# Performance work log

Hardware: AMD Instinct MI355X
Metric: run time of the kernel (lower is better)

The kernel has to match this reference:

```python
import jax, jax.numpy as jnp
import numpy as np

B, T, D, H, K = 2, 1024, 1024, 4096, 8


def setup_inputs() -> dict:
    key = jax.random.key(0)
    ks = jax.random.split(key, 5)
    x = jax.random.normal(ks[0], (B, T, D), dtype=jnp.float32)
    # hard one-hot routing weights per token (no learned router)
    expert_ids = jax.random.randint(ks[1], (B, T), 0, K)
    combine_weights = jax.nn.one_hot(expert_ids, K, dtype=jnp.float32)
    scale_in = 1.0 / np.sqrt(D)
    scale_h = 1.0 / np.sqrt(H)
    wg = jax.random.normal(ks[2], (K, D, H), dtype=jnp.float32) * scale_in
    wu = jax.random.normal(ks[3], (K, D, H), dtype=jnp.float32) * scale_in
    wd = jax.random.normal(ks[4], (K, H, D), dtype=jnp.float32) * scale_h
    return {"x": x, "combine_weights": combine_weights, "wg": wg, "wu": wu, "wd": wd}


def reference(x, combine_weights, wg, wu, wd):
    # Each expert is a SwiGLU FFN: down( silu(gate(x)) * up(x) ).
    # Dense baseline: every token runs through all K experts (as in source).
    g = jnp.einsum('btd,kdh->btkh', x, wg)          # [B,T,K,H]
    u = jnp.einsum('btd,kdh->btkh', x, wu)          # [B,T,K,H]
    h = jax.nn.silu(g) * u                          # [B,T,K,H]
    expert_outs = jnp.einsum('btkh,khd->btkd', h, wd)  # [B,T,K,D]
    y = jnp.einsum('btk,btkd->btd', combine_weights, expert_outs)
    return y.astype(x.dtype)
```

## Files before the change

### kernel.cpp

```cpp
#include <hip/hip_runtime.h>

typedef __attribute__((ext_vector_type(8))) short bf16x8;
typedef __attribute__((ext_vector_type(4))) float f32x4;
typedef unsigned short u16;

#define NTOK 2048
#define DDIM 1024
#define HDIM 4096
#define KEXP 8

#define BM 320
#define BK 64
#define NDESC 16

__device__ __forceinline__ u16 f2bf(float f) {
  union { float f; unsigned int u; } c; c.f = f;
  unsigned int u = c.u;
  return (u16)((u + 0x7FFFu + ((u >> 16) & 1u)) >> 16);
}
__device__ __forceinline__ unsigned pk2(float a, float b) {
  return (unsigned)f2bf(a) | ((unsigned)f2bf(b) << 16);
}

#define BAR() do { \
  asm volatile("s_waitcnt lgkmcnt(0)" ::: "memory"); \
  __builtin_amdgcn_sched_barrier(0); \
  __builtin_amdgcn_s_barrier(); \
  __builtin_amdgcn_sched_barrier(0); \
} while (0)

__global__ void route_kernel(const float* __restrict__ cw, int* __restrict__ offs,
                             int* __restrict__ perm, float* __restrict__ wsel,
                             int* __restrict__ desc) {
  __shared__ int cnt[KEXP];
  __shared__ int base[KEXP];
  const int t = threadIdx.x;
  if (t < KEXP) cnt[t] = 0;
  __syncthreads();
  int eid[8]; float wv[8];
  #pragma unroll
  for (int i = 0; i < 8; i++) {
    const int tok = t * 8 + i;
    const float* p = cw + tok * KEXP;
    int best = 0; float bw = p[0];
    #pragma unroll
    for (int k = 1; k < KEXP; k++) { float v = p[k]; if (v > bw) { bw = v; best = k; } }
    eid[i] = best; wv[i] = bw;
    atomicAdd(&cnt[best], 1);
  }
  __syncthreads();
  if (t == 0) {
    int s = 0, nd = 0;
    for (int k = 0; k < KEXP; k++) {
      const int ck = cnt[k];
      base[k] = s; offs[k] = s;
      for (int m0 = 0; m0 < ck && nd < NDESC; m0 += BM)
        desc[nd++] = (k << 12) | (s + m0);
      s += ck;
    }
    offs[KEXP] = s;
    for (; nd < NDESC; nd++) desc[nd] = -1;
  }
  __syncthreads();
  #pragma unroll
  for (int i = 0; i < 8; i++) {
    const int tok = t * 8 + i;
    const int pos = atomicAdd(&base[eid[i]], 1);
    perm[pos] = tok;
    wsel[pos] = wv[i];
  }
}

__global__ void gather_x(const float* __restrict__ x, const int* __restrict__ perm,
                         u16* __restrict__ Xb) {
  const int slot = blockIdx.x;
  const int tok = perm[slot];
  const int t = threadIdx.x;
  float4 v = ((const float4*)(x + (size_t)tok * DDIM))[t];
  ushort4 o; o.x = f2bf(v.x); o.y = f2bf(v.y); o.z = f2bf(v.z); o.w = f2bf(v.w);
  ((ushort4*)(Xb + (size_t)slot * DDIM))[t] = o;
}

__global__ __launch_bounds__(1024, 4) void gemm_swiglu(
    const u16* __restrict__ Xb,
    const float* __restrict__ wg, const float* __restrict__ wu,
    const int* __restrict__ offs, const int* __restrict__ desc,
    u16* __restrict__ Hb) {
  __shared__ u16 As[2][BM * 64];
  __shared__ u16 Bs[2][2][64 * 64];

  const int d = desc[blockIdx.y];
  if (d < 0) return;
  const int e = d >> 12;
  const int slot0 = d & 0xFFF;
  const int Msub = offs[e + 1] - slot0;
  const int n0 = blockIdx.x * 64;

  const int t = threadIdx.x;
  const int lane = t & 63;
  const int W = t >> 6;
  const int wm = W >> 2;
  const int wn = W & 3;
  const int l15 = lane & 15;
  const int lhi = lane >> 4;

  const bool do_a = t < 640;
  const int a_row = t >> 1;
  const int a_c0 = (t & 1) * 4;
  const u16* a_src = Xb + (size_t)min(slot0 + a_row, NTOK - 1) * DDIM + a_c0 * 8;
  const int a_swz = a_row & 7;

  const int tb = t & 511;
  const int matsel = t >> 9;
  const float* b_base = (matsel ? wu : wg) + (size_t)e * DDIM * HDIM;
  const int b_n = tb & 63;
  const int b_c = tb >> 6;
  const float* b_src = b_base + (size_t)(b_c * 8) * HDIM + n0 + b_n;
  const int b_off = b_n * 64 + ((b_c ^ (b_n & 7)) << 3);

  float bR[8];
  f32x4 accg[5] = {};
  f32x4 accu[5] = {};

  #define LOADB(tile) { const float* p_ = b_src + (size_t)(tile) * BK * HDIM; \
    _Pragma("unroll") for (int j = 0; j < 8; j++) bR[j] = p_[(size_t)j * HDIM]; }
  #define WRITEB(buf) { uint4 w_; \
    w_.x = pk2(bR[0], bR[1]); w_.y = pk2(bR[2], bR[3]); \
    w_.z = pk2(bR[4], bR[5]); w_.w = pk2(bR[6], bR[7]); \
    *(uint4*)(&Bs[buf][matsel][b_off]) = w_; }
  #define STAGE(buf, tA, tBnext, doB) { \
    uint4 a0_ = {}, a1_ = {}, a2_ = {}, a3_ = {}; \
    if (do_a) { const uint4* p_ = (const uint4*)(a_src + (tA) * BK); \
      a0_ = p_[0]; a1_ = p_[1]; a2_ = p_[2]; a3_ = p_[3]; } \
    WRITEB(buf); \
    if (doB) LOADB(tBnext); \
    if (do_a) { u16* base_ = &As[buf][a_row * 64]; \
      *(uint4*)(base_ + (((a_c0 + 0) ^ a_swz) << 3)) = a0_; \
      *(uint4*)(base_ + (((a_c0 + 1) ^ a_swz) << 3)) = a1_; \
      *(uint4*)(base_ + (((a_c0 + 2) ^ a_swz) << 3)) = a2_; \
      *(uint4*)(base_ + (((a_c0 + 3) ^ a_swz) << 3)) = a3_; } \
  }
  #define COMPUTE(buf) { _Pragma("unroll") for (int ks = 0; ks < 2; ks++) { \
      const int cx_ = (((ks << 2) + lhi) ^ (l15 & 7)) << 3; \
      bf16x8 bg_ = *(const bf16x8*)(&Bs[buf][0][(wn * 16 + l15) * 64] + cx_); \
      bf16x8 bu_ = *(const bf16x8*)(&Bs[buf][1][(wn * 16 + l15) * 64] + cx_); \
      _Pragma("unroll") for (int fm = 0; fm < 5; fm++) { \
        bf16x8 af_ = *(const bf16x8*)(&As[buf][(wm * 80 + fm * 16 + l15) * 64] + cx_); \
        accg[fm] = __builtin_amdgcn_mfma_f32_16x16x32_bf16(af_, bg_, accg[fm], 0, 0, 0); \
        accu[fm] = __builtin_amdgcn_mfma_f32_16x16x32_bf16(af_, bu_, accu[fm], 0, 0, 0); } } }

  LOADB(0);
  STAGE(0, 0, 1, true);
  BAR();

  #pragma unroll 1
  for (int it = 0; it < 16; it += 2) {
    if (it + 1 < 16) STAGE(1, it + 1, it + 2, (it + 2 < 16));
    COMPUTE(0);
    BAR();
    if (it + 2 < 16) STAGE(0, it + 2, it + 3, (it + 3 < 16));
    COMPUTE(1);
    BAR();
  }
  #undef LOADB
  #undef WRITEB
  #undef STAGE
  #undef COMPUTE

  #pragma unroll
  for (int fm = 0; fm < 5; fm++) {
    #pragma unroll
    for (int i = 0; i < 4; i++) {
      const int row = wm * 80 + fm * 16 + lhi * 4 + i;
      if (row < Msub) {
        const float g = accg[fm][i];
        const float u = accu[fm][i];
        const float h = (g / (1.0f + __expf(-g))) * u;
        Hb[(size_t)(slot0 + row) * HDIM + n0 + wn * 16 + l15] = f2bf(h);
      }
    }
  }
}

__global__ __launch_bounds__(1024, 4) void gemm_down(
    const u16* __restrict__ Hb, const float* __restrict__ wd,
    const int* __restrict__ offs, const int* __restrict__ desc,
    const int* __restrict__ perm, const float* __restrict__ wsel,
    float* __restrict__ y) {
  __shared__ u16 As[2][BM * 64];
  __shared__ u16 Bs[2][128 * 64];

  const int d = desc[blockIdx.y];
  if (d < 0) return;
  const int e = d >> 12;
  const int slot0 = d & 0xFFF;
  const int Msub = offs[e + 1] - slot0;
  const int n0 = blockIdx.x * 128;
  const int kbase = blockIdx.z * (HDIM / 4);

  const float* Wd = wd + (size_t)e * HDIM * DDIM;

  const int t = threadIdx.x;
  const int lane = t & 63;
  const int W = t >> 6;
  const int wm = W >> 2;
  const int wn = W & 3;
  const int l15 = lane & 15;
  const int lhi = lane >> 4;

  const bool do_a = t < 640;
  const int a_row = t >> 1;
  const int a_c0 = (t & 1) * 4;
  const u16* a_src = Hb + (size_t)min(slot0 + a_row, NTOK - 1) * HDIM + kbase + a_c0 * 8;
  const int a_swz = a_row & 7;

  const int b_n = t & 127;
  const int b_c = t >> 7;
  const float* b_src = Wd + (size_t)(kbase + b_c * 8) * DDIM + n0 + b_n;
  const int b_off = b_n * 64 + ((b_c ^ (b_n & 7)) << 3);

  float bR[8];
  f32x4 acc[5][2] = {};

  #define LOADB(tile) { const float* p_ = b_src + (size_t)(tile) * BK * DDIM; \
    _Pragma("unroll") for (int j = 0; j < 8; j++) bR[j] = p_[(size_t)j * DDIM]; }
  #define WRITEB(buf) { uint4 w_; \
    w_.x = pk2(bR[0], bR[1]); w_.y = pk2(bR[2], bR[3]); \
    w_.z = pk2(bR[4], bR[5]); w_.w = pk2(bR[6], bR[7]); \
    *(uint4*)(&Bs[buf][b_off]) = w_; }
  #define STAGE(buf, tA, tBnext, doB) { \
    uint4 a0_ = {}, a1_ = {}, a2_ = {}, a3_ = {}; \
    if (do_a) { const uint4* p_ = (const uint4*)(a_src + (tA) * BK); \
      a0_ = p_[0]; a1_ = p_[1]; a2_ = p_[2]; a3_ = p_[3]; } \
    WRITEB(buf); \
    if (doB) LOADB(tBnext); \
    if (do_a) { u16* base_ = &As[buf][a_row * 64]; \
      *(uint4*)(base_ + (((a_c0 + 0) ^ a_swz) << 3)) = a0_; \
      *(uint4*)(base_ + (((a_c0 + 1) ^ a_swz) << 3)) = a1_; \
      *(uint4*)(base_ + (((a_c0 + 2) ^ a_swz) << 3)) = a2_; \
      *(uint4*)(base_ + (((a_c0 + 3) ^ a_swz) << 3)) = a3_; } \
  }
  #define COMPUTE(buf) { _Pragma("unroll") for (int ks = 0; ks < 2; ks++) { \
      const int cx_ = (((ks << 2) + lhi) ^ (l15 & 7)) << 3; \
      bf16x8 bf0_ = *(const bf16x8*)(&Bs[buf][(wn * 32 + l15) * 64] + cx_); \
      bf16x8 bf1_ = *(const bf16x8*)(&Bs[buf][(wn * 32 + 16 + l15) * 64] + cx_); \
      _Pragma("unroll") for (int fm = 0; fm < 5; fm++) { \
        bf16x8 af_ = *(const bf16x8*)(&As[buf][(wm * 80 + fm * 16 + l15) * 64] + cx_); \
        acc[fm][0] = __builtin_amdgcn_mfma_f32_16x16x32_bf16(af_, bf0_, acc[fm][0], 0, 0, 0); \
        acc[fm][1] = __builtin_amdgcn_mfma_f32_16x16x32_bf16(af_, bf1_, acc[fm][1], 0, 0, 0); } } }

  LOADB(0);
  STAGE(0, 0, 1, true);
  BAR();

  #pragma unroll 1
  for (int it = 0; it < 16; it += 2) {
    if (it + 1 < 16) STAGE(1, it + 1, it + 2, (it + 2 < 16));
    COMPUTE(0);
    BAR();
    if (it + 2 < 16) STAGE(0, it + 2, it + 3, (it + 3 < 16));
    COMPUTE(1);
    BAR();
  }
  #undef LOADB
  #undef WRITEB
  #undef STAGE
  #undef COMPUTE

  #pragma unroll
  for (int fm = 0; fm < 5; fm++) {
    #pragma unroll
    for (int i = 0; i < 4; i++) {
      const int row = wm * 80 + fm * 16 + lhi * 4 + i;
      if (row < Msub) {
        const int slot = slot0 + row;
        const int tok = perm[slot];
        const float w = wsel[slot];
        const size_t base = (size_t)tok * DDIM + n0 + wn * 32;
        atomicAdd(y + base + l15, acc[fm][0][i] * w);
        atomicAdd(y + base + 16 + l15, acc[fm][1][i] * w);
      }
    }
  }
}

extern "C" void kernel_launch(void* const* d_in, const int* in_sizes, int n_in,
                              void* d_out, int out_size, void* d_ws, size_t ws_size,
                              hipStream_t stream) {
  const float* x  = (const float*)d_in[0];
  const float* cw = (const float*)d_in[1];
  const float* wg = (const float*)d_in[2];
  const float* wu = (const float*)d_in[3];
  const float* wd = (const float*)d_in[4];
  float* y = (float*)d_out;

  char* ws = (char*)d_ws;
  int* offs   = (int*)ws;
  int* desc   = (int*)(ws + 64);
  int* perm   = (int*)(ws + 128);
  float* wsel = (float*)(ws + 128 + NTOK * 4);
  u16* Xb = (u16*)(ws + 32768);
  u16* Hb = (u16*)(ws + 32768 + (size_t)NTOK * DDIM * 2);

  hipMemsetAsync(d_out, 0, (size_t)NTOK * DDIM * sizeof(float), stream);
  route_kernel<<<1, 256, 0, stream>>>(cw, offs, perm, wsel, desc);
  gather_x<<<NTOK, 256, 0, stream>>>(x, perm, Xb);
  gemm_swiglu<<<dim3(HDIM / 64, NDESC), 1024, 0, stream>>>(Xb, wg, wu, offs, desc, Hb);
  gemm_down<<<dim3(DDIM / 128, NDESC, 4), 1024, 0, stream>>>(Hb, wd, offs, desc, perm, wsel, y);
}
```

Measured before the change: 163.3 us.

## Load A fragments directly from global, halve N tiles and block size

Result: slower. 302.8 us (+85.5%).

```diff
diff --git a/kernel.cpp b/kernel.cpp
--- a/kernel.cpp
+++ b/kernel.cpp
@@ -1,4 +1,5 @@
 #include <hip/hip_runtime.h>
+#include <hip/hip_bf16.h>
 
 typedef __attribute__((ext_vector_type(8))) short bf16x8;
 typedef __attribute__((ext_vector_type(4))) float f32x4;
@@ -14,9 +15,8 @@
 #define NDESC 16
 
 __device__ __forceinline__ u16 f2bf(float f) {
-  union { float f; unsigned int u; } c; c.f = f;
-  unsigned int u = c.u;
-  return (u16)((u + 0x7FFFu + ((u >> 16) & 1u)) >> 16);
+  __hip_bfloat16 b = __float2bfloat16(f);
+  union { __hip_bfloat16 b; u16 u; } c; c.b = b; return c.u;
 }
 __device__ __forceinline__ unsigned pk2(float a, float b) {
   return (unsigned)f2bf(a) | ((unsigned)f2bf(b) << 16);
@@ -81,40 +81,38 @@
   ((ushort4*)(Xb + (size_t)slot * DDIM))[t] = o;
 }
 
-__global__ __launch_bounds__(1024, 4) void gemm_swiglu(
+__global__ __launch_bounds__(512, 4) void gemm_swiglu(
     const u16* __restrict__ Xb,
     const float* __restrict__ wg, const float* __restrict__ wu,
     const int* __restrict__ offs, const int* __restrict__ desc,
     u16* __restrict__ Hb) {
-  __shared__ u16 As[2][BM * 64];
-  __shared__ u16 Bs[2][2][64 * 64];
+  __shared__ u16 Bs[2][2][32 * 64];
 
   const int d = desc[blockIdx.y];
   if (d < 0) return;
   const int e = d >> 12;
   const int slot0 = d & 0xFFF;
   const int Msub = offs[e + 1] - slot0;
-  const int n0 = blockIdx.x * 64;
+  const int n0 = blockIdx.x * 32;
 
   const int t = threadIdx.x;
   const int lane = t & 63;
   const int W = t >> 6;
-  const int wm = W >> 2;
-  const int wn = W & 3;
+  const int wm = W >> 1;
+  const int wn = W & 1;
   const int l15 = lane & 15;
   const int lhi = lane >> 4;
 
-  const bool do_a = t < 640;
-  const int a_row = t >> 1;
-  const int a_c0 = (t & 1) * 4;
-  const u16* a_src = Xb + (size_t)min(slot0 + a_row, NTOK - 1) * DDIM + a_c0 * 8;
-  const int a_swz = a_row & 7;
-
-  const int tb = t & 511;
-  const int matsel = t >> 9;
+  const u16* aP[5];
+  #pragma unroll
+  for (int fm = 0; fm < 5; fm++)
+    aP[fm] = Xb + (size_t)min(slot0 + wm * 80 + fm * 16 + l15, NTOK - 1) * DDIM + lhi * 8;
+
+  const int tb = t & 255;
+  const int matsel = t >> 8;
   const float* b_base = (matsel ? wu : wg) + (size_t)e * DDIM * HDIM;
-  const int b_n = tb & 63;
-  const int b_c = tb >> 6;
+  const int b_n = tb & 31;
+  const int b_c = tb >> 5;
   const float* b_src = b_base + (size_t)(b_c * 8) * HDIM + n0 + b_n;
   const int b_off = b_n * 64 + ((b_c ^ (b_n & 7)) << 3);
 
@@ -128,43 +126,33 @@
     w_.x = pk2(bR[0], bR[1]); w_.y = pk2(bR[2], bR[3]); \
     w_.z = pk2(bR[4], bR[5]); w_.w = pk2(bR[6], bR[7]); \
     *(uint4*)(&Bs[buf][matsel][b_off]) = w_; }
-  #define STAGE(buf, tA, tBnext, doB) { \
-    uint4 a0_ = {}, a1_ = {}, a2_ = {}, a3_ = {}; \
-    if (do_a) { const uint4* p_ = (const uint4*)(a_src + (tA) * BK); \
-      a0_ = p_[0]; a1_ = p_[1]; a2_ = p_[2]; a3_ = p_[3]; } \
-    WRITEB(buf); \
-    if (doB) LOADB(tBnext); \
-    if (do_a) { u16* base_ = &As[buf][a_row * 64]; \
-      *(uint4*)(base_ + (((a_c0 + 0) ^ a_swz) << 3)) = a0_; \
-      *(uint4*)(base_ + (((a_c0 + 1) ^ a_swz) << 3)) = a1_; \
-      *(uint4*)(base_ + (((a_c0 + 2) ^ a_swz) << 3)) = a2_; \
-      *(uint4*)(base_ + (((a_c0 + 3) ^ a_swz) << 3)) = a3_; } \
-  }
-  #define COMPUTE(buf) { _Pragma("unroll") for (int ks = 0; ks < 2; ks++) { \
+  #define COMPUTE(buf, itv) { _Pragma("unroll") for (int ks = 0; ks < 2; ks++) { \
       const int cx_ = (((ks << 2) + lhi) ^ (l15 & 7)) << 3; \
       bf16x8 bg_ = *(const bf16x8*)(&Bs[buf][0][(wn * 16 + l15) * 64] + cx_); \
       bf16x8 bu_ = *(const bf16x8*)(&Bs[buf][1][(wn * 16 + l15) * 64] + cx_); \
+      const int ao_ = (itv) * 64 + ks * 32; \
       _Pragma("unroll") for (int fm = 0; fm < 5; fm++) { \
-        bf16x8 af_ = *(const bf16x8*)(&As[buf][(wm * 80 + fm * 16 + l15) * 64] + cx_); \
+        bf16x8 af_ = *(const bf16x8*)(aP[fm] + ao_); \
         accg[fm] = __builtin_amdgcn_mfma_f32_16x16x32_bf16(af_, bg_, accg[fm], 0, 0, 0); \
         accu[fm] = __builtin_amdgcn_mfma_f32_16x16x32_bf16(af_, bu_, accu[fm], 0, 0, 0); } } }
 
   LOADB(0);
-  STAGE(0, 0, 1, true);
+  WRITEB(0);
+  LOADB(1);
   BAR();
 
   #pragma unroll 1
   for (int it = 0; it < 16; it += 2) {
-    if (it + 1 < 16) STAGE(1, it + 1, it + 2, (it + 2 < 16));
-    COMPUTE(0);
-    BAR();
-    if (it + 2 < 16) STAGE(0, it + 2, it + 3, (it + 3 < 16));
-    COMPUTE(1);
+    WRITEB(1);
+    if (it + 2 < 16) LOADB(it + 2);
+    COMPUTE(0, it);
+    BAR();
+    if (it + 2 < 16) { WRITEB(0); if (it + 3 < 16) LOADB(it + 3); }
+    COMPUTE(1, it + 1);
     BAR();
   }
   #undef LOADB
   #undef WRITEB
-  #undef STAGE
   #undef COMPUTE
 
   #pragma unroll
@@ -182,20 +170,19 @@
   }
 }
 
-__global__ __launch_bounds__(1024, 4) void gemm_down(
+__global__ __launch_bounds__(512, 4) void gemm_down(
     const u16* __restrict__ Hb, const float* __restrict__ wd,
     const int* __restrict__ offs, const int* __restrict__ desc,
     const int* __restrict__ perm, const float* __restrict__ wsel,
     float* __restrict__ y) {
-  __shared__ u16 As[2][BM * 64];
-  __shared__ u16 Bs[2][128 * 64];
+  __shared__ u16 Bs[2][64 * 64];
 
   const int d = desc[blockIdx.y];
   if (d < 0) return;
   const int e = d >> 12;
   const int slot0 = d & 0xFFF;
   const int Msub = offs[e + 1] - slot0;
-  const int n0 = blockIdx.x * 128;
+  const int n0 = blockIdx.x * 64;
   const int kbase = blockIdx.z * (HDIM / 4);
 
   const float* Wd = wd + (size_t)e * HDIM * DDIM;
@@ -203,19 +190,18 @@
   const int t = threadIdx.x;
   const int lane = t & 63;
   const int W = t >> 6;
-  const int wm = W >> 2;
-  const int wn = W & 3;
+  const int wm = W >> 1;
+  const int wn = W & 1;
   const int l15 = lane & 15;
   const int lhi = lane >> 4;
 
-  const bool do_a = t < 640;
-  const int a_row = t >> 1;
-  const int a_c0 = (t & 1) * 4;
-  const u16* a_src = Hb + (size_t)min(slot0 + a_row, NTOK - 1) * HDIM + kbase + a_c0 * 8;
-  const int a_swz = a_row & 7;
-
-  const int b_n = t & 127;
-  const int b_c = t >> 7;
+  const u16* aP[5];
+  #pragma unroll
+  for (int fm = 0; fm < 5; fm++)
+    aP[fm] = Hb + (size_t)min(slot0 + wm * 80 + fm * 16 + l15, NTOK - 1) * HDIM + kbase + lhi * 8;
+
+  const int b_n = t & 63;
+  const int b_c = t >> 6;
   const float* b_src = Wd + (size_t)(kbase + b_c * 8) * DDIM + n0 + b_n;
   const int b_off = b_n * 64 + ((b_c ^ (b_n & 7)) << 3);
 
@@ -228,43 +214,33 @@
     w_.x = pk2(bR[0], bR[1]); w_.y = pk2(bR[2], bR[3]); \
     w_.z = pk2(bR[4], bR[5]); w_.w = pk2(bR[6], bR[7]); \
     *(uint4*)(&Bs[buf][b_off]) = w_; }
-  #define STAGE(buf, tA, tBnext, doB) { \
-    uint4 a0_ = {}, a1_ = {}, a2_ = {}, a3_ = {}; \
-    if (do_a) { const uint4* p_ = (const uint4*)(a_src + (tA) * BK); \
-      a0_ = p_[0]; a1_ = p_[1]; a2_ = p_[2]; a3_ = p_[3]; } \
-    WRITEB(buf); \
-    if (doB) LOADB(tBnext); \
-    if (do_a) { u16* base_ = &As[buf][a_row * 64]; \
-      *(uint4*)(base_ + (((a_c0 + 0) ^ a_swz) << 3)) = a0_; \
-      *(uint4*)(base_ + (((a_c0 + 1) ^ a_swz) << 3)) = a1_; \
-      *(uint4*)(base_ + (((a_c0 + 2) ^ a_swz) << 3)) = a2_; \
-      *(uint4*)(base_ + (((a_c0 + 3) ^ a_swz) << 3)) = a3_; } \
-  }
-  #define COMPUTE(buf) { _Pragma("unroll") for (int ks = 0; ks < 2; ks++) { \
+  #define COMPUTE(buf, itv) { _Pragma("unroll") for (int ks = 0; ks < 2; ks++) { \
       const int cx_ = (((ks << 2) + lhi) ^ (l15 & 7)) << 3; \
       bf16x8 bf0_ = *(const bf16x8*)(&Bs[buf][(wn * 32 + l15) * 64] + cx_); \
       bf16x8 bf1_ = *(const bf16x8*)(&Bs[buf][(wn * 32 + 16 + l15) * 64] + cx_); \
+      const int ao_ = (itv) * 64 + ks * 32; \
       _Pragma("unroll") for (int fm = 0; fm < 5; fm++) { \
-        bf16x8 af_ = *(const bf16x8*)(&As[buf][(wm * 80 + fm * 16 + l15) * 64] + cx_); \
+        bf16x8 af_ = *(const bf16x8*)(aP[fm] + ao_); \
         acc[fm][0] = __builtin_amdgcn_mfma_f32_16x16x32_bf16(af_, bf0_, acc[fm][0], 0, 0, 0); \
         acc[fm][1] = __builtin_amdgcn_mfma_f32_16x16x32_bf16(af_, bf1_, acc[fm][1], 0, 0, 0); } } }
 
   LOADB(0);
-  STAGE(0, 0, 1, true);
+  WRITEB(0);
+  LOADB(1);
   BAR();
 
   #pragma unroll 1
   for (int it = 0; it < 16; it += 2) {
-    if (it + 1 < 16) STAGE(1, it + 1, it + 2, (it + 2 < 16));
-    COMPUTE(0);
-    BAR();
-    if (it + 2 < 16) STAGE(0, it + 2, it + 3, (it + 3 < 16));
-    COMPUTE(1);
+    WRITEB(1);
+    if (it + 2 < 16) LOADB(it + 2);
+    COMPUTE(0, it);
+    BAR();
+    if (it + 2 < 16) { WRITEB(0); if (it + 3 < 16) LOADB(it + 3); }
+    COMPUTE(1, it + 1);
     BAR();
   }
   #undef LOADB
   #undef WRITEB
-  #undef STAGE
   #undef COMPUTE
 
   #pragma unroll
@@ -305,6 +281,6 @@
   hipMemsetAsync(d_out, 0, (size_t)NTOK * DDIM * sizeof(float), stream);
   route_kernel<<<1, 256, 0, stream>>>(cw, offs, perm, wsel, desc);
   gather_x<<<NTOK, 256, 0, stream>>>(x, perm, Xb);
-  gemm_swiglu<<<dim3(HDIM / 64, NDESC), 1024, 0, stream>>>(Xb, wg, wu, offs, desc, Hb);
-  gemm_down<<<dim3(DDIM / 128, NDESC, 4), 1024, 0, stream>>>(Hb, wd, offs, desc, perm, wsel, y);
-}
+  gemm_swiglu<<<dim3(HDIM / 32, NDESC), 512, 0, stream>>>(Xb, wg, wu, offs, desc, Hb);
+  gemm_down<<<dim3(DDIM / 64, NDESC, 4), 512, 0, stream>>>(Hb, wd, offs, desc, perm, wsel, y);
+}
```
